# Optimization experiments

Measured on AMD Instinct MI355X. Metric: run time of the kernel, lower is better.

The kernel has to match this reference:

```python
import jax, jax.numpy as jnp
import numpy as np

NUM_IDS = 8
K_HALF = 5            # k = K//2
DIM = 2048
CP_DIM = DIM // 8     # cp_ratio = 8
N = NUM_IDS * 2 * K_HALF
H, W = 24, 8


def _kaiming(key, out_c, in_c):
    # kaiming_normal_(fan_out, relu) for a 1x1 conv: std = sqrt(2/out_c)
    return jax.random.normal(key, (out_c, in_c), dtype=jnp.float32) * np.sqrt(2.0 / out_c)


def setup_inputs() -> dict:
    key = jax.random.key(0)
    ks = jax.random.split(key, 8)
    inputs = jax.random.normal(ks[0], (N, DIM, H, W), dtype=jnp.float32)
    # PK batch: each identity has K_HALF samples with sub==1 and K_HALF with sub==0
    labels = jnp.repeat(jnp.arange(NUM_IDS, dtype=jnp.int64), 2 * K_HALF)
    sub = jnp.tile(jnp.concatenate([jnp.ones(K_HALF, jnp.int64), jnp.zeros(K_HALF, jnp.int64)]), NUM_IDS)
    return {
        "inputs": inputs,
        "labels": labels,
        "sub": sub,
        "W_ri": _kaiming(ks[1], CP_DIM, DIM),
        "W_rv": _kaiming(ks[2], CP_DIM, DIM),
        "W_ci": _kaiming(ks[3], DIM, K_HALF * CP_DIM),
        "W_cv": _kaiming(ks[4], DIM, K_HALF * CP_DIM),
        "W_f": _kaiming(ks[5], DIM, 2 * DIM),
    }


def reference(inputs, labels, sub, W_ri, W_rv, W_ci, W_cv, W_f):
    n, c, h, w = inputs.shape
    cp = W_ri.shape[0]
    k = W_ci.shape[1] // cp
    n_half = n // 2
    x = jax.lax.stop_gradient(inputs)  # .detach() in the original

    def branch(sub_mask_val, Wr, Wc):
        # indices of samples in this sub-group (order-preserving, like boolean mask)
        sidx = jnp.nonzero(sub == sub_mask_val, size=n_half)[0]
        xs = jnp.einsum('nchw,oc->nohw', x[sidx], Wr)       # [n_half, cp, h, w]
        lab = labels[sidx]                                   # [n_half]
        # for each batch sample, the k positions in the sub-group with matching label
        match = labels[:, None] == lab[None, :]              # [n, n_half]
        pos = jnp.where(match, jnp.arange(n_half)[None, :], n_half)
        gidx = jnp.sort(pos, axis=1)[:, :k]                  # [n, k]
        aff = xs[gidx].reshape(n, k * cp, h, w)              # gather + channel-stack
        return jax.nn.relu(jnp.einsum('nchw,oc->nohw', aff, Wc))

    s_i = branch(1, W_ri, W_ci)   # sub == 1
    s_v = branch(0, W_rv, W_cv)   # sub == 0
    x_fuse = jax.nn.sigmoid(
        jnp.einsum('nchw,oc->nohw', jnp.concatenate([s_i, s_v], axis=1), W_f))
    return inputs + inputs * x_fuse
```

## Files before the change

### kernel.cpp

```cpp
#include <hip/hip_runtime.h>

typedef unsigned short u16;
typedef unsigned int u32;
typedef __bf16 bf16_t;
typedef bf16_t bf16x8 __attribute__((ext_vector_type(8)));
typedef float f32x16 __attribute__((ext_vector_type(16)));

#define DIM 2048
#define HW  192
#define CP  256
#define NB  80

__device__ __forceinline__ u16 f2b(float f) {
    u32 u = __float_as_uint(f);
    u32 r = (u + 0x7FFFu + ((u >> 16) & 1u)) >> 16;
    return (u16)r;
}

__device__ __forceinline__ void g2l16(const void* g, void* l) {
    __builtin_amdgcn_global_load_lds(
        (const __attribute__((address_space(1))) u32*)g,
        (__attribute__((address_space(3))) u32*)l, 16, 0, 0);
}

template<int ACT, bool OUTF32, typename F>
__device__ __forceinline__ void gemm_core(F actAddr, int arstride,
    const u16* __restrict__ Wp, int wstride, int K,
    void* __restrict__ outp, int M)
{
    __shared__ u16 act_s[2][96 * 32];
    __shared__ u16 w_s[2][128 * 32];
    const int t    = threadIdx.x;
    const int w    = t >> 6;
    const int lane = t & 63;
    const int ln   = lane & 31;
    const int q2   = lane >> 5;
    const int swz  = (ln >> 1) & 3;

    f32x16 acc[3][2];
    #pragma unroll
    for (int i = 0; i < 3; ++i)
        #pragma unroll
        for (int j = 0; j < 2; ++j)
            #pragma unroll
            for (int r = 0; r < 16; ++r) acc[i][j][r] = 0.f;

    auto stage = [&](int buf, int k0) {
        const u16* ap = actAddr(k0);
        #pragma unroll
        for (int r = 0; r < 4; ++r) {
            int idx = r * 128 + t;
            int row = idx >> 2, pc = idx & 3;
            int lc  = pc ^ ((row >> 1) & 3);
            g2l16(Wp + (size_t)row * wstride + k0 + lc * 8, (void*)(w_s[buf] + idx * 8));
        }
        #pragma unroll
        for (int r = 0; r < 3; ++r) {
            int idx = r * 128 + t;
            int row = idx >> 2, pc = idx & 3;
            int lc  = pc ^ ((row >> 1) & 3);
            g2l16(ap + (size_t)row * arstride + lc * 8, (void*)(act_s[buf] + idx * 8));
        }
    };

    auto compute = [&](int buf) {
        #pragma unroll
        for (int s = 0; s < 2; ++s) {
            bf16x8 af[3], bf[2];
            const int phys = (s * 2 + q2) ^ swz;
            #pragma unroll
            for (int i = 0; i < 3; ++i)
                af[i] = *(const bf16x8*)(act_s[buf] + (i * 32 + ln) * 32 + phys * 8);
            #pragma unroll
            for (int j = 0; j < 2; ++j)
                bf[j] = *(const bf16x8*)(w_s[buf] + (w * 64 + j * 32 + ln) * 32 + phys * 8);
            #pragma unroll
            for (int i = 0; i < 3; ++i)
                #pragma unroll
                for (int j = 0; j < 2; ++j)
                    acc[i][j] = __builtin_amdgcn_mfma_f32_32x32x16_bf16(
                        af[i], bf[j], acc[i][j], 0, 0, 0);
        }
    };

    stage(0, 0);
    const int iters = K / 32;
    for (int it = 0; it < iters; ++it) {
        int b = it & 1;
        __syncthreads();
        if (it + 1 < iters) stage(b ^ 1, (it + 1) * 32);
        compute(b);
    }

    #pragma unroll
    for (int i = 0; i < 3; ++i) {
        #pragma unroll
        for (int j = 0; j < 2; ++j) {
            #pragma unroll
            for (int r = 0; r < 16; ++r) {
                float v = acc[i][j][r];
                if (ACT == 1) v = v > 0.f ? v : 0.f;
                int nl = i * 32 + (r & 3) + 8 * (r >> 2) + 4 * q2;
                int ml = w * 64 + j * 32 + ln;
                if (OUTF32) ((float*)outp)[(size_t)nl * M + ml] = v;
                else        ((u16*)outp)[(size_t)nl * M + ml] = f2b(v);
            }
        }
    }
}

__global__ __launch_bounds__(128) void proj_g(const u16* __restrict__ xt,
    const int* __restrict__ sub, int nbase,
    const u16* __restrict__ Wri, const u16* __restrict__ Wrv,
    u16* __restrict__ projt)
{
    const int z = blockIdx.z, bn = blockIdx.x, bm = blockIdx.y;
    const int n = nbase + z;
    const u16* act = xt + (size_t)z * (HW * DIM) + (size_t)bn * 96 * DIM;
    const u16* Wp  = ((sub[n] != 0) ? Wri : Wrv) + (size_t)bm * 128 * DIM;
    u16* outp = projt + (size_t)n * (HW * CP) + (size_t)(bn * 96) * CP + bm * 128;
    auto f = [=](int k0) { return act + k0; };
    gemm_core<0, false>(f, DIM, Wp, DIM, DIM, outp, CP);
}

__global__ __launch_bounds__(128) void compose_g(const u16* __restrict__ projt,
    const u16* __restrict__ Wci, const u16* __restrict__ Wcv,
    u16* __restrict__ st)
{
    const int z = blockIdx.z, br = z >> 3, id = z & 7;
    const int bn = blockIdx.x, bm = blockIdx.y;
    const u16* base = projt + (size_t)(id * 10 + br * 5) * (HW * CP) + (size_t)bn * 96 * CP;
    const u16* Wp   = (br ? Wcv : Wci) + (size_t)bm * 128 * 1280;
    u16* outp = st + (size_t)(id * 2 + br) * (HW * DIM) + (size_t)bn * 96 * DIM + bm * 128;
    auto f = [=](int k0) { return base + (size_t)(k0 >> 8) * (HW * CP) + (k0 & 255); };
    gemm_core<1, false>(f, CP, Wp, 1280, 1280, outp, DIM);
}

__global__ __launch_bounds__(128) void fuse_g(const u16* __restrict__ st,
    const u16* __restrict__ Wf, float* __restrict__ fuset4)
{
    const int z = blockIdx.z, h = z >> 3, id = z & 7;
    const int bn = blockIdx.x, bm = blockIdx.y;
    const u16* base = st + (size_t)(id * 2 + (h >> 1)) * (HW * DIM)
                    + (size_t)bn * 96 * DIM + (h & 1) * 1024;
    const u16* Wp   = Wf + (size_t)bm * 128 * (2 * DIM) + (size_t)h * 1024;
    float* outp = fuset4 + (size_t)h * (8 * HW * DIM) + (size_t)id * (HW * DIM)
                + (size_t)bn * 96 * DIM + bm * 128;
    auto f = [=](int k0) { return base + k0; };
    gemm_core<0, true>(f, DIM, Wp, 2 * DIM, 1024, outp, DIM);
}

__global__ __launch_bounds__(256) void xt_k(const float* __restrict__ x,
                                            u16* __restrict__ xt)
{
    __shared__ float ts[64][65];
    const int z = blockIdx.z;
    const int p0 = blockIdx.x * 64, c0 = blockIdx.y * 64;
    const int t = threadIdx.x;
    #pragma unroll
    for (int r = 0; r < 4; ++r) {
        int idx = r * 256 + t;
        int c = idx >> 4, p4 = (idx & 15) * 4;
        float4 v = *(const float4*)(x + ((size_t)z * DIM + c0 + c) * HW + p0 + p4);
        ts[c][p4 + 0] = v.x; ts[c][p4 + 1] = v.y;
        ts[c][p4 + 2] = v.z; ts[c][p4 + 3] = v.w;
    }
    __syncthreads();
    #pragma unroll
    for (int r = 0; r < 4; ++r) {
        int idx = r * 256 + t;
        int p = idx >> 4, c4 = (idx & 15) * 4;
        ushort4 o;
        o.x = f2b(ts[c4 + 0][p]); o.y = f2b(ts[c4 + 1][p]);
        o.z = f2b(ts[c4 + 2][p]); o.w = f2b(ts[c4 + 3][p]);
        *(ushort4*)(xt + ((size_t)z * HW + p0 + p) * DIM + c0 + c4) = o;
    }
}

__global__ __launch_bounds__(256) void fuse_tr(const float* __restrict__ fuset4,
                                               float* __restrict__ fuse)
{
    __shared__ float ts[64][65];
    const int id = blockIdx.z;
    const int c0 = blockIdx.x * 64, p0 = blockIdx.y * 64;
    const int t = threadIdx.x, l = t & 63;
    const size_t hs = (size_t)8 * HW * DIM;
    #pragma unroll
    for (int i = 0; i < 16; ++i) {
        int pl = (t >> 6) * 16 + i;
        size_t a = ((size_t)id * HW + p0 + pl) * DIM + c0 + l;
        float v = fuset4[a] + fuset4[a + hs] + fuset4[a + 2 * hs] + fuset4[a + 3 * hs];
        ts[pl][l] = 1.f / (1.f + __expf(-v));
    }
    __syncthreads();
    #pragma unroll
    for (int i = 0; i < 16; ++i) {
        int cl = (t >> 6) * 16 + i;
        fuse[((size_t)id * DIM + c0 + cl) * HW + p0 + l] = ts[l][cl];
    }
}

__global__ __launch_bounds__(256) void wcvt(
    const float* __restrict__ a0, const float* __restrict__ a1,
    const float* __restrict__ a2, const float* __restrict__ a3,
    const float* __restrict__ a4,
    u16* __restrict__ o0, u16* __restrict__ o1, u16* __restrict__ o2,
    u16* __restrict__ o3, u16* __restrict__ o4)
{
    size_t off = ((size_t)blockIdx.x * 256 + threadIdx.x) * 4;
    const float* s; u16* d;
    if (off < 524288)                    { s = a0; d = o0; }
    else if ((off -= 524288) < 524288)   { s = a1; d = o1; }
    else if ((off -= 524288) < 2621440)  { s = a2; d = o2; }
    else if ((off -= 2621440) < 2621440) { s = a3; d = o3; }
    else                                 { off -= 2621440; s = a4; d = o4; }
    float4 v = *(const float4*)(s + off);
    ushort4 p;
    p.x = f2b(v.x); p.y = f2b(v.y); p.z = f2b(v.z); p.w = f2b(v.w);
    *(ushort4*)(d + off) = p;
}

__global__ __launch_bounds__(256) void final_kernel(const float* __restrict__ x,
    const int* __restrict__ labels, const float* __restrict__ fusebuf,
    float* __restrict__ out)
{
    const u32 e = ((u32)blockIdx.x * 256u + threadIdx.x) * 4u;
    const u32 n   = e / ((u32)DIM * HW);
    const u32 rem = e % ((u32)DIM * HW);
    const int id  = labels[n];
    float4 xv = *reinterpret_cast<const float4*>(x + e);
    float4 fv = *reinterpret_cast<const float4*>(fusebuf + (size_t)id * DIM * HW + rem);
    float4 o;
    o.x = xv.x + xv.x * fv.x;
    o.y = xv.y + xv.y * fv.y;
    o.z = xv.z + xv.z * fv.z;
    o.w = xv.w + xv.w * fv.w;
    *reinterpret_cast<float4*>(out + e) = o;
}

extern "C" void kernel_launch(void* const* d_in, const int* in_sizes, int n_in,
                              void* d_out, int out_size, void* d_ws, size_t ws_size,
                              hipStream_t stream) {
    const float* x      = (const float*)d_in[0];
    const int*   labels = (const int*)d_in[1];
    const int*   sub    = (const int*)d_in[2];
    const float* Wri    = (const float*)d_in[3];
    const float* Wrv    = (const float*)d_in[4];
    const float* Wci    = (const float*)d_in[5];
    const float* Wcv    = (const float*)d_in[6];
    const float* Wf     = (const float*)d_in[7];
    float* out = (float*)d_out;
    char* ws = (char*)d_ws;

    const bool full = ws_size >= (size_t)175636480;
    const size_t xtb = full ? (size_t)62914560 : (size_t)15728640;

    u16* Wri_b = (u16*)(ws);
    u16* Wrv_b = (u16*)(ws + 1048576);
    u16* Wci_b = (u16*)(ws + 2097152);
    u16* Wcv_b = (u16*)(ws + 7340032);
    u16* Wf_b  = (u16*)(ws + 12582912);
    u16* xtbuf = (u16*)(ws + 29360128);
    u16* projt = (u16*)(ws + 29360128 + xtb);
    u16* stb   = (u16*)(ws + 29360128 + xtb + 7864320);
    float* fuset4 = (float*)(ws + 29360128 + xtb + 7864320 + 12582912);
    float* fuse   = (float*)(ws + 29360128 + xtb + 7864320 + 12582912 + 50331648);

    wcvt<<<14336, 256, 0, stream>>>(Wri, Wrv, Wci, Wcv, Wf,
                                    Wri_b, Wrv_b, Wci_b, Wcv_b, Wf_b);
    const int nchunk = full ? 1 : 4;
    const int cs = NB / nchunk;
    for (int c = 0; c < nchunk; ++c) {
        xt_k  <<<dim3(3, 32, cs), 256, 0, stream>>>(x + (size_t)c * cs * DIM * HW, xtbuf);
        proj_g<<<dim3(2, 2, cs), 128, 0, stream>>>(xtbuf, sub, c * cs, Wri_b, Wrv_b, projt);
    }
    compose_g<<<dim3(2, 16, 16), 128, 0, stream>>>(projt, Wci_b, Wcv_b, stb);
    fuse_g   <<<dim3(2, 16, 32), 128, 0, stream>>>(stb, Wf_b, fuset4);
    fuse_tr  <<<dim3(32, 3, 8), 256, 0, stream>>>(fuset4, fuse);
    final_kernel<<<30720, 256, 0, stream>>>(x, labels, fuse, out);
}
```

Baseline: 450.9 us.

## Split-K the projection GEMM four ways with a separate fp32 reduction kernel

The projection GEMM previously launched only 2x2xNB blocks, each running the full K=2048 reduction. It now splits K into four 512-wide slices, quadrupling the grid to raise occupancy. Each slice writes fp32 partials into a reused workspace buffer, and a new reduction kernel sums them and converts to bf16. This trades an extra launch and extra fp32 memory traffic for more parallelism.

```diff
diff --git a/kernel.cpp b/kernel.cpp
--- a/kernel.cpp
+++ b/kernel.cpp
@@ -112,15 +112,34 @@
 __global__ __launch_bounds__(128) void proj_g(const u16* __restrict__ xt,
     const int* __restrict__ sub, int nbase,
     const u16* __restrict__ Wri, const u16* __restrict__ Wrv,
-    u16* __restrict__ projt)
-{
-    const int z = blockIdx.z, bn = blockIdx.x, bm = blockIdx.y;
+    float* __restrict__ proj4)
+{
+    const int zz = blockIdx.z, z = zz >> 2, p = zz & 3;
+    const int bn = blockIdx.x, bm = blockIdx.y;
     const int n = nbase + z;
-    const u16* act = xt + (size_t)z * (HW * DIM) + (size_t)bn * 96 * DIM;
-    const u16* Wp  = ((sub[n] != 0) ? Wri : Wrv) + (size_t)bm * 128 * DIM;
-    u16* outp = projt + (size_t)n * (HW * CP) + (size_t)(bn * 96) * CP + bm * 128;
+    const u16* act = xt + (size_t)z * (HW * DIM) + (size_t)bn * 96 * DIM + p * 512;
+    const u16* Wp  = ((sub[n] != 0) ? Wri : Wrv) + (size_t)bm * 128 * DIM + p * 512;
+    float* outp = proj4 + (size_t)p * ((size_t)NB * HW * CP)
+                + (size_t)n * (HW * CP) + (size_t)(bn * 96) * CP + bm * 128;
     auto f = [=](int k0) { return act + k0; };
-    gemm_core<0, false>(f, DIM, Wp, DIM, DIM, outp, CP);
+    gemm_core<0, true>(f, DIM, Wp, DIM, 512, outp, CP);
+}
+
+__global__ __launch_bounds__(256) void proj_red(const float* __restrict__ proj4,
+                                                u16* __restrict__ projt)
+{
+    const size_t i = ((size_t)blockIdx.x * 256 + threadIdx.x) * 4;
+    const size_t S = (size_t)NB * HW * CP;
+    float4 a = *(const float4*)(proj4 + i);
+    float4 b = *(const float4*)(proj4 + i + S);
+    float4 c = *(const float4*)(proj4 + i + 2 * S);
+    float4 d = *(const float4*)(proj4 + i + 3 * S);
+    ushort4 o;
+    o.x = f2b(a.x + b.x + c.x + d.x);
+    o.y = f2b(a.y + b.y + c.y + d.y);
+    o.z = f2b(a.z + b.z + c.z + d.z);
+    o.w = f2b(a.w + b.w + c.w + d.w);
+    *(ushort4*)(projt + i) = o;
 }
 
 __global__ __launch_bounds__(128) void compose_g(const u16* __restrict__ projt,
@@ -265,6 +284,7 @@
     u16* stb   = (u16*)(ws + 29360128 + xtb + 7864320);
     float* fuset4 = (float*)(ws + 29360128 + xtb + 7864320 + 12582912);
     float* fuse   = (float*)(ws + 29360128 + xtb + 7864320 + 12582912 + 50331648);
+    float* proj4 = fuset4;
 
     wcvt<<<14336, 256, 0, stream>>>(Wri, Wrv, Wci, Wcv, Wf,
                                     Wri_b, Wrv_b, Wci_b, Wcv_b, Wf_b);
@@ -272,8 +292,9 @@
     const int cs = NB / nchunk;
     for (int c = 0; c < nchunk; ++c) {
         xt_k  <<<dim3(3, 32, cs), 256, 0, stream>>>(x + (size_t)c * cs * DIM * HW, xtbuf);
-        proj_g<<<dim3(2, 2, cs), 128, 0, stream>>>(xtbuf, sub, c * cs, Wri_b, Wrv_b, projt);
-    }
+        proj_g<<<dim3(2, 2, cs * 4), 128, 0, stream>>>(xtbuf, sub, c * cs, Wri_b, Wrv_b, proj4);
+    }
+    proj_red<<<3840, 256, 0, stream>>>(proj4, projt);
     compose_g<<<dim3(2, 16, 16), 128, 0, stream>>>(projt, Wci_b, Wcv_b, stb);
     fuse_g   <<<dim3(2, 16, 32), 128, 0, stream>>>(stb, Wf_b, fuset4);
     fuse_tr  <<<dim3(32, 3, 8), 256, 0, stream>>>(fuset4, fuse);
```

New measurement: 441.5 us. -2.1%, faster.
